# Kernel optimization log

Hardware: AMD Instinct MI355X
Metric: run time of the kernel (lower is better)

## Reference

```python
import math
import jax, jax.numpy as jnp
import numpy as np

B, S, D = 16, 2048, 256

def setup_inputs() -> dict:
    key = jax.random.key(0)
    kq, kk, kv, km = jax.random.split(key, 4)
    q = jax.random.normal(kq, (B, S, D), dtype=jnp.float32)
    k = jax.random.normal(kk, (B, S, D), dtype=jnp.float32)
    v = jax.random.normal(kv, (B, S, D), dtype=jnp.float32)
    mask = jax.random.randint(km, (B, S, S), 0, 2, dtype=jnp.int32)
    return {"q": q, "k": k, "v": v, "mask": mask}

def reference(q, k, v, mask):
    dim_input = q.shape[-1]
    # scores: [B, S, S]
    scores = jnp.einsum('bqd,bkd->bqk', q, k) / math.sqrt(dim_input)
    # non-standard masking: masked positions set to 0.0 (NOT -inf) before softmax
    scores = jnp.where(mask == 0, jnp.float32(0.0), scores)
    att = jax.nn.softmax(scores, axis=-1)
    # original: if mask.sum() == 0, attention is all zeros
    att = jnp.where(mask.sum() > 0, att, jnp.zeros_like(att))
    return jnp.einsum('bqk,bkd->bqd', att, v)
```

## Files before the change

### kernel.cpp

```cpp
#include <hip/hip_runtime.h>


#define B_  16
#define S_  2048
#define D_  256
#define KT  32
#define NT_ 64
#define TILE_BYTES 16384

typedef short bf16x8 __attribute__((ext_vector_type(8)));
typedef float f32x4  __attribute__((ext_vector_type(4)));

__device__ __forceinline__ unsigned short f2bf(float x) {
    union { float f; unsigned u; } c; c.f = x;
    unsigned u = c.u;
    u += 0x7FFFu + ((u >> 16) & 1u);
    return (unsigned short)(u >> 16);
}

#define GLDS(g, l) __builtin_amdgcn_global_load_lds( \
    (const __attribute__((address_space(1))) void*)(g), \
    (__attribute__((address_space(3))) void*)(l), 16, 0, 0)

__global__ void conv_k(const float* __restrict__ k, char* __restrict__ kbf) {
    const int gid = blockIdx.x * 256 + threadIdx.x;
    const int d8  = gid & 31;
    const int kv  = (gid >> 5) & 2047;
    const int b   = gid >> 16;
    const float* src = k + (((size_t)(b * S_ + kv)) << 8) + d8 * 8;
    const float4 f0 = *(const float4*)src;
    const float4 f1 = *(const float4*)(src + 4);
    bf16x8 h;
    h[0] = (short)f2bf(f0.x); h[1] = (short)f2bf(f0.y);
    h[2] = (short)f2bf(f0.z); h[3] = (short)f2bf(f0.w);
    h[4] = (short)f2bf(f1.x); h[5] = (short)f2bf(f1.y);
    h[6] = (short)f2bf(f1.z); h[7] = (short)f2bf(f1.w);
    const int tile = kv >> 5, kvl = kv & 31;
    char* dst = kbf + (((size_t)(b * NT_ + tile)) << 14)
                    + (kvl << 9) + ((d8 * 16) ^ ((kvl & 7) << 4));
    *(bf16x8*)dst = h;
}

__global__ void conv_vt(const float* __restrict__ v, char* __restrict__ vtbf) {
    const int gid  = blockIdx.x * 256 + threadIdx.x;
    const int d    = gid & 255;
    const int g    = (gid >> 8) & 3;
    const int tile = (gid >> 10) & 63;
    const int b    = gid >> 16;
    const int kv0  = tile * KT + g * 8;
    const float* src = v + (((size_t)(b * S_ + kv0)) << 8) + d;
    bf16x8 h;
    #pragma unroll
    for (int j = 0; j < 8; ++j) h[j] = (short)f2bf(src[(size_t)j << 8]);
    char* dst = vtbf + (((size_t)(b * NT_ + tile)) << 14)
                     + (d << 6) + ((g * 16) ^ (((d >> 1) & 3) << 4));
    *(bf16x8*)dst = h;
}

__global__ __launch_bounds__(256, 1)
void attn_main(const float* __restrict__ q, const int* __restrict__ mask,
               const char* __restrict__ kbf, const char* __restrict__ vtbf,
               float* __restrict__ out)
{
    __shared__ alignas(128) char lds[73728];

    const int tid  = threadIdx.x;
    const int wid  = tid >> 6;
    const int lane = tid & 63;
    const int ln15 = lane & 15;
    const int quad = lane >> 4;
    const int swzK = (ln15 & 7) << 4;
    const int swzA = ((ln15 >> 1) & 3) << 4;

    const int bid = blockIdx.x;
    const int bx  = (bid & 7) * 32 + (bid >> 3);
    const int b   = bx >> 4;
    const int qt  = bx & 15;
    const int qw  = qt * 128 + wid * 32;

    const float QS = 0.09016844f;
    bf16x8 aq[2][8];
    #pragma unroll
    for (int s = 0; s < 2; ++s) {
        const float* qrow = q + ((size_t)(b * S_ + qw + s * 16 + ln15)) * D_;
        #pragma unroll
        for (int ks = 0; ks < 8; ++ks) {
            const float4 f0 = *(const float4*)(qrow + ks * 32 + quad * 8);
            const float4 f1 = *(const float4*)(qrow + ks * 32 + quad * 8 + 4);
            bf16x8 a;
            a[0] = (short)f2bf(f0.x * QS); a[1] = (short)f2bf(f0.y * QS);
            a[2] = (short)f2bf(f0.z * QS); a[3] = (short)f2bf(f0.w * QS);
            a[4] = (short)f2bf(f1.x * QS); a[5] = (short)f2bf(f1.y * QS);
            a[6] = (short)f2bf(f1.z * QS); a[7] = (short)f2bf(f1.w * QS);
            aq[s][ks] = a;
        }
    }

    bf16x8 ones;
    #pragma unroll
    for (int e = 0; e < 8; ++e) ones[e] = (short)0x3F80;

    f32x4 oacc[2][16];
    #pragma unroll
    for (int s = 0; s < 2; ++s)
        #pragma unroll
        for (int i = 0; i < 16; ++i) oacc[s][i] = (f32x4){0.f, 0.f, 0.f, 0.f};
    f32x4 lacc[2];
    lacc[0] = (f32x4){0.f, 0.f, 0.f, 0.f};
    lacc[1] = (f32x4){0.f, 0.f, 0.f, 0.f};

    const char* ktile = kbf  + (((size_t)b * NT_) << 14);
    const char* vtile = vtbf + (((size_t)b * NT_) << 14);
    char* pw = lds + 65536 + wid * 2048;
    const int c0 = wid * 4;

    #pragma unroll
    for (int c = 0; c < 4; ++c) {
        GLDS(ktile + (c0 + c) * 1024 + lane * 16, lds +         (c0 + c) * 1024);
        GLDS(vtile + (c0 + c) * 1024 + lane * 16, lds + 32768 + (c0 + c) * 1024);
    }

    const int* mbase = mask + ((size_t)(b * S_ + qw + 4 * quad)) * S_;
    int mcur[16], mnext[16];
    #pragma unroll
    for (int s = 0; s < 2; ++s)
        #pragma unroll
        for (int nt = 0; nt < 2; ++nt)
            #pragma unroll
            for (int r = 0; r < 4; ++r)
                mcur[s * 8 + nt * 4 + r] =
                    mbase[(size_t)(s * 16 + r) * S_ + nt * 16 + ln15];

    for (int t = 0; t < NT_; ++t) {
        const int cur = t & 1;
        __syncthreads();

        if (t + 1 < NT_) {
            const char* kg = ktile + ((size_t)(t + 1) << 14);
            const char* vg = vtile + ((size_t)(t + 1) << 14);
            const int nb = cur ^ 1;
            #pragma unroll
            for (int c = 0; c < 4; ++c) {
                GLDS(kg + (c0 + c) * 1024 + lane * 16, lds + nb * 16384 +         (c0 + c) * 1024);
                GLDS(vg + (c0 + c) * 1024 + lane * 16, lds + 32768 + nb * 16384 + (c0 + c) * 1024);
            }
            const int kv2 = (t + 1) * KT;
            #pragma unroll
            for (int s = 0; s < 2; ++s)
                #pragma unroll
                for (int nt = 0; nt < 2; ++nt)
                    #pragma unroll
                    for (int r = 0; r < 4; ++r)
                        mnext[s * 8 + nt * 4 + r] =
                            mbase[(size_t)(s * 16 + r) * S_ + kv2 + nt * 16 + ln15];
        }

        const char* kl = lds + cur * 16384;
        f32x4 sacc[2][2];
        sacc[0][0] = (f32x4){0.f, 0.f, 0.f, 0.f};
        sacc[0][1] = (f32x4){0.f, 0.f, 0.f, 0.f};
        sacc[1][0] = (f32x4){0.f, 0.f, 0.f, 0.f};
        sacc[1][1] = (f32x4){0.f, 0.f, 0.f, 0.f};
        #pragma unroll
        for (int ks = 0; ks < 8; ++ks) {
            #pragma unroll
            for (int nt = 0; nt < 2; ++nt) {
                const int off = ((nt * 16 + ln15) << 9)
                              + (((ks << 6) + (quad << 4)) ^ swzK);
                const bf16x8 bk = *(const bf16x8*)(kl + off);
                sacc[0][nt] = __builtin_amdgcn_mfma_f32_16x16x32_bf16(aq[0][ks], bk, sacc[0][nt], 0, 0, 0);
                sacc[1][nt] = __builtin_amdgcn_mfma_f32_16x16x32_bf16(aq[1][ks], bk, sacc[1][nt], 0, 0, 0);
            }
        }

        #pragma unroll
        for (int s = 0; s < 2; ++s) {
            #pragma unroll
            for (int nt = 0; nt < 2; ++nt) {
                #pragma unroll
                for (int r = 0; r < 4; ++r) {
                    const float p = (mcur[s * 8 + nt * 4 + r] != 0)
                                  ? exp2f(sacc[s][nt][r]) : 1.0f;
                    const int row  = s * 16 + 4 * quad + r;
                    const int boff = (row << 6)
                                   + ((nt * 32 + ln15 * 2) ^ (((row >> 1) & 3) << 4));
                    *(unsigned short*)(pw + boff) = f2bf(p);
                }
            }
        }

        const bf16x8 ap0 = *(const bf16x8*)(pw + (ln15 << 6)        + ((quad << 4) ^ swzA));
        const bf16x8 ap1 = *(const bf16x8*)(pw + ((16 + ln15) << 6) + ((quad << 4) ^ swzA));
        lacc[0] = __builtin_amdgcn_mfma_f32_16x16x32_bf16(ap0, ones, lacc[0], 0, 0, 0);
        lacc[1] = __builtin_amdgcn_mfma_f32_16x16x32_bf16(ap1, ones, lacc[1], 0, 0, 0);
        const char* vl = lds + 32768 + cur * 16384;
        #pragma unroll
        for (int nt2 = 0; nt2 < 16; ++nt2) {
            const int voff = ((nt2 * 16 + ln15) << 6) + ((quad << 4) ^ swzA);
            const bf16x8 bv = *(const bf16x8*)(vl + voff);
            oacc[0][nt2] = __builtin_amdgcn_mfma_f32_16x16x32_bf16(ap0, bv, oacc[0][nt2], 0, 0, 0);
            oacc[1][nt2] = __builtin_amdgcn_mfma_f32_16x16x32_bf16(ap1, bv, oacc[1][nt2], 0, 0, 0);
        }

        if (t + 1 < NT_) {
            #pragma unroll
            for (int i = 0; i < 16; ++i) mcur[i] = mnext[i];
        }
    }

    #pragma unroll
    for (int s = 0; s < 2; ++s) {
        #pragma unroll
        for (int r = 0; r < 4; ++r) {
            const float inv = 1.0f / lacc[s][r];
            float* orow = out + ((size_t)(b * S_ + qw + s * 16 + 4 * quad + r)) * D_ + ln15;
            #pragma unroll
            for (int nt2 = 0; nt2 < 16; ++nt2)
                orow[nt2 * 16] = oacc[s][nt2][r] * inv;
        }
    }
}

#define QT 128
#define KTF 64
#define NW 8
#define KSTR 264
#define VSTR 72
#define PSTR 72

__global__ __launch_bounds__(512, 2)
void attn_fused_v1(const float* __restrict__ q, const float* __restrict__ k,
                   const float* __restrict__ v, const int* __restrict__ mask,
                   float* __restrict__ out)
{
    __shared__ unsigned short Kl[KTF * KSTR];
    __shared__ unsigned short Vt[D_ * VSTR];
    __shared__ unsigned short Pl[NW][16 * PSTR];

    const int tid  = threadIdx.x;
    const int wid  = tid >> 6;
    const int lane = tid & 63;
    const int ln15 = lane & 15;
    const int quad = lane >> 4;
    const int bid = blockIdx.x;
    const int bx  = (bid & 7) * 32 + (bid >> 3);
    const int b  = bx >> 4;
    const int qt = bx & 15;
    const int qw = qt * QT + wid * 16;

    const float* qb = q + ((size_t)b * S_ + qw) * D_;
    const float* kb = k + (size_t)b * S_ * D_;
    const float* vb = v + (size_t)b * S_ * D_;
    const int*   mb = mask + ((size_t)b * S_ + qw) * (size_t)S_;

    bf16x8 aq[8];
    {
        const float* qrow = qb + (size_t)ln15 * D_;
        #pragma unroll
        for (int ks = 0; ks < 8; ++ks) {
            const float4 f0 = *(const float4*)(qrow + ks * 32 + quad * 8);
            const float4 f1 = *(const float4*)(qrow + ks * 32 + quad * 8 + 4);
            bf16x8 a;
            a[0] = (short)f2bf(f0.x * 0.0625f); a[1] = (short)f2bf(f0.y * 0.0625f);
            a[2] = (short)f2bf(f0.z * 0.0625f); a[3] = (short)f2bf(f0.w * 0.0625f);
            a[4] = (short)f2bf(f1.x * 0.0625f); a[5] = (short)f2bf(f1.y * 0.0625f);
            a[6] = (short)f2bf(f1.z * 0.0625f); a[7] = (short)f2bf(f1.w * 0.0625f);
            aq[ks] = a;
        }
    }
    bf16x8 ones;
    #pragma unroll
    for (int e = 0; e < 8; ++e) ones[e] = (short)0x3F80;
    f32x4 oacc[16];
    #pragma unroll
    for (int i = 0; i < 16; ++i) oacc[i] = (f32x4){0.f, 0.f, 0.f, 0.f};
    f32x4 lacc = (f32x4){0.f, 0.f, 0.f, 0.f};
    const int kst_c0 = (tid & 63) * 4;

    for (int kt2 = 0; kt2 < S_ / KTF; ++kt2) {
        const int kvbase = kt2 * KTF;
        int mval[4][4];
        #pragma unroll
        for (int nt = 0; nt < 4; ++nt)
            #pragma unroll
            for (int r = 0; r < 4; ++r)
                mval[nt][r] = mb[(size_t)(4 * quad + r) * S_ + kvbase + nt * 16 + ln15];
        __syncthreads();
        {
            const float* ks_ = kb + (size_t)kvbase * D_;
            #pragma unroll
            for (int pass = 0; pass < 8; ++pass) {
                const int r = pass * 8 + wid;
                const float4 f = *(const float4*)(ks_ + (size_t)r * D_ + kst_c0);
                ushort4 h;
                h.x = f2bf(f.x); h.y = f2bf(f.y); h.z = f2bf(f.z); h.w = f2bf(f.w);
                *(ushort4*)&Kl[r * KSTR + kst_c0] = h;
            }
        }
        {
            const float* vs_ = vb + (size_t)kvbase * D_;
            #pragma unroll
            for (int pass = 0; pass < 8; ++pass) {
                const int idx = pass * 8 + wid;
                const int kv  = (idx & 3) * 16 + ln15;
                const int d0  = (idx >> 2) * 16 + 4 * quad;
                const float4 f = *(const float4*)(vs_ + (size_t)kv * D_ + d0);
                Vt[(d0 + 0) * VSTR + kv] = f2bf(f.x);
                Vt[(d0 + 1) * VSTR + kv] = f2bf(f.y);
                Vt[(d0 + 2) * VSTR + kv] = f2bf(f.z);
                Vt[(d0 + 3) * VSTR + kv] = f2bf(f.w);
            }
        }
        __syncthreads();
        f32x4 sacc[4];
        #pragma unroll
        for (int nt = 0; nt < 4; ++nt) sacc[nt] = (f32x4){0.f, 0.f, 0.f, 0.f};
        #pragma unroll
        for (int ks = 0; ks < 8; ++ks) {
            #pragma unroll
            for (int nt = 0; nt < 4; ++nt) {
                const bf16x8 bk =
                    *(const bf16x8*)&Kl[(nt * 16 + ln15) * KSTR + ks * 32 + quad * 8];
                sacc[nt] = __builtin_amdgcn_mfma_f32_16x16x32_bf16(aq[ks], bk, sacc[nt], 0, 0, 0);
            }
        }
        unsigned short* pwv = Pl[wid];
        #pragma unroll
        for (int nt = 0; nt < 4; ++nt) {
            #pragma unroll
            for (int r = 0; r < 4; ++r) {
                const float s = sacc[nt][r];
                const float p = (mval[nt][r] != 0) ? __expf(s) : 1.0f;
                pwv[(4 * quad + r) * PSTR + nt * 16 + ln15] = f2bf(p);
            }
        }
        #pragma unroll
        for (int ks2 = 0; ks2 < 2; ++ks2) {
            const bf16x8 ap = *(const bf16x8*)&pwv[ln15 * PSTR + ks2 * 32 + quad * 8];
            lacc = __builtin_amdgcn_mfma_f32_16x16x32_bf16(ap, ones, lacc, 0, 0, 0);
            #pragma unroll
            for (int nt2 = 0; nt2 < 16; ++nt2) {
                const bf16x8 bv =
                    *(const bf16x8*)&Vt[(nt2 * 16 + ln15) * VSTR + ks2 * 32 + quad * 8];
                oacc[nt2] = __builtin_amdgcn_mfma_f32_16x16x32_bf16(ap, bv, oacc[nt2], 0, 0, 0);
            }
        }
    }
    #pragma unroll
    for (int r = 0; r < 4; ++r) {
        const float inv = 1.0f / lacc[r];
        float* orow = out + ((size_t)b * S_ + qw + 4 * quad + r) * D_ + ln15;
        #pragma unroll
        for (int nt2 = 0; nt2 < 16; ++nt2)
            orow[nt2 * 16] = oacc[nt2][r] * inv;
    }
}

extern "C" void kernel_launch(void* const* d_in, const int* in_sizes, int n_in,
                              void* d_out, int out_size, void* d_ws, size_t ws_size,
                              hipStream_t stream) {
    const float* q    = (const float*)d_in[0];
    const float* k    = (const float*)d_in[1];
    const float* v    = (const float*)d_in[2];
    const int*   mask = (const int*)d_in[3];
    float*       out  = (float*)d_out;

    const size_t one = (size_t)B_ * NT_ * TILE_BYTES;
    if (ws_size >= 2 * one) {
        char* kbf  = (char*)d_ws;
        char* vtbf = kbf + one;
        conv_k <<<4096, 256, 0, stream>>>(k, kbf);
        conv_vt<<<4096, 256, 0, stream>>>(v, vtbf);
        attn_main<<<256, 256, 0, stream>>>(q, mask, kbf, vtbf, out);
    } else {
        attn_fused_v1<<<512, 512, 0, stream>>>(q, k, v, mask, out);
    }
}
```

Baseline: 182.5 us.

## Split KV tile across two wave groups with LDS reduction of partial outputs

```diff
diff --git a/kernel.cpp b/kernel.cpp
--- a/kernel.cpp
+++ b/kernel.cpp
@@ -4,9 +4,8 @@
 #define B_  16
 #define S_  2048
 #define D_  256
-#define KT  32
-#define NT_ 64
-#define TILE_BYTES 16384
+#define NPH 32
+#define TILE_BYTES 32768
 
 typedef short bf16x8 __attribute__((ext_vector_type(8)));
 typedef float f32x4  __attribute__((ext_vector_type(4)));
@@ -35,48 +34,50 @@
     h[2] = (short)f2bf(f0.z); h[3] = (short)f2bf(f0.w);
     h[4] = (short)f2bf(f1.x); h[5] = (short)f2bf(f1.y);
     h[6] = (short)f2bf(f1.z); h[7] = (short)f2bf(f1.w);
-    const int tile = kv >> 5, kvl = kv & 31;
-    char* dst = kbf + (((size_t)(b * NT_ + tile)) << 14)
+    const int tile = kv >> 6, kvl = kv & 63;
+    char* dst = kbf + (((size_t)(b * NPH + tile)) << 15)
                     + (kvl << 9) + ((d8 * 16) ^ ((kvl & 7) << 4));
     *(bf16x8*)dst = h;
 }
 
 __global__ void conv_vt(const float* __restrict__ v, char* __restrict__ vtbf) {
     const int gid  = blockIdx.x * 256 + threadIdx.x;
-    const int d    = gid & 255;
-    const int g    = (gid >> 8) & 3;
-    const int tile = (gid >> 10) & 63;
+    const int kg   = gid & 7;
+    const int d    = (gid >> 3) & 255;
+    const int tile = (gid >> 11) & 31;
     const int b    = gid >> 16;
-    const int kv0  = tile * KT + g * 8;
+    const int kv0  = tile * 64 + kg * 8;
     const float* src = v + (((size_t)(b * S_ + kv0)) << 8) + d;
     bf16x8 h;
     #pragma unroll
     for (int j = 0; j < 8; ++j) h[j] = (short)f2bf(src[(size_t)j << 8]);
-    char* dst = vtbf + (((size_t)(b * NT_ + tile)) << 14)
-                     + (d << 6) + ((g * 16) ^ (((d >> 1) & 3) << 4));
+    char* dst = vtbf + (((size_t)(b * NPH + tile)) << 15)
+                     + (d << 7) + ((kg * 16) ^ ((d & 7) << 4));
     *(bf16x8*)dst = h;
 }
 
-__global__ __launch_bounds__(256, 1)
+__global__ __launch_bounds__(512, 2)
 void attn_main(const float* __restrict__ q, const int* __restrict__ mask,
                const char* __restrict__ kbf, const char* __restrict__ vtbf,
                float* __restrict__ out)
 {
-    __shared__ alignas(128) char lds[73728];
+    __shared__ alignas(128) char lds[147456];
 
     const int tid  = threadIdx.x;
     const int wid  = tid >> 6;
     const int lane = tid & 63;
     const int ln15 = lane & 15;
     const int quad = lane >> 4;
+    const int g    = wid & 3;
+    const int h    = wid >> 2;
     const int swzK = (ln15 & 7) << 4;
-    const int swzA = ((ln15 >> 1) & 3) << 4;
+    const int swzP = ((ln15 >> 1) & 3) << 4;
 
     const int bid = blockIdx.x;
     const int bx  = (bid & 7) * 32 + (bid >> 3);
     const int b   = bx >> 4;
     const int qt  = bx & 15;
-    const int qw  = qt * 128 + wid * 32;
+    const int qw  = qt * 128 + g * 32;
 
     const float QS = 0.09016844f;
     bf16x8 aq[2][8];
@@ -109,42 +110,46 @@
     lacc[0] = (f32x4){0.f, 0.f, 0.f, 0.f};
     lacc[1] = (f32x4){0.f, 0.f, 0.f, 0.f};
 
-    const char* ktile = kbf  + (((size_t)b * NT_) << 14);
-    const char* vtile = vtbf + (((size_t)b * NT_) << 14);
-    char* pw = lds + 65536 + wid * 2048;
-    const int c0 = wid * 4;
+    const char* ktile = kbf  + (((size_t)b * NPH) << 15);
+    const char* vtile = vtbf + (((size_t)b * NPH) << 15);
+    char* pw = lds + 131072 + wid * 2048;
+    const int cK = wid * 4;
+    const int cV = wid * 4;
 
     #pragma unroll
     for (int c = 0; c < 4; ++c) {
-        GLDS(ktile + (c0 + c) * 1024 + lane * 16, lds +         (c0 + c) * 1024);
-        GLDS(vtile + (c0 + c) * 1024 + lane * 16, lds + 32768 + (c0 + c) * 1024);
+        GLDS(ktile + (cK + c) * 1024 + lane * 16, lds + (cK + c) * 1024);
+        GLDS(vtile + (cV + c) * 1024 + lane * 16, lds + 65536 + (cV + c) * 1024);
     }
 
     const int* mbase = mask + ((size_t)(b * S_ + qw + 4 * quad)) * S_;
     int mcur[16], mnext[16];
-    #pragma unroll
-    for (int s = 0; s < 2; ++s)
-        #pragma unroll
-        for (int nt = 0; nt < 2; ++nt)
-            #pragma unroll
-            for (int r = 0; r < 4; ++r)
-                mcur[s * 8 + nt * 4 + r] =
-                    mbase[(size_t)(s * 16 + r) * S_ + nt * 16 + ln15];
-
-    for (int t = 0; t < NT_; ++t) {
-        const int cur = t & 1;
+    {
+        const int kvb = h * 32;
+        #pragma unroll
+        for (int s = 0; s < 2; ++s)
+            #pragma unroll
+            for (int nt = 0; nt < 2; ++nt)
+                #pragma unroll
+                for (int r = 0; r < 4; ++r)
+                    mcur[s * 8 + nt * 4 + r] =
+                        mbase[(size_t)(s * 16 + r) * S_ + kvb + nt * 16 + ln15];
+    }
+
+    for (int ph = 0; ph < NPH; ++ph) {
+        const int cur = ph & 1;
         __syncthreads();
 
-        if (t + 1 < NT_) {
-            const char* kg = ktile + ((size_t)(t + 1) << 14);
-            const char* vg = vtile + ((size_t)(t + 1) << 14);
+        if (ph + 1 < NPH) {
+            const char* kg_ = ktile + ((size_t)(ph + 1) << 15);
+            const char* vg_ = vtile + ((size_t)(ph + 1) << 15);
             const int nb = cur ^ 1;
             #pragma unroll
             for (int c = 0; c < 4; ++c) {
-                GLDS(kg + (c0 + c) * 1024 + lane * 16, lds + nb * 16384 +         (c0 + c) * 1024);
-                GLDS(vg + (c0 + c) * 1024 + lane * 16, lds + 32768 + nb * 16384 + (c0 + c) * 1024);
-            }
-            const int kv2 = (t + 1) * KT;
+                GLDS(kg_ + (cK + c) * 1024 + lane * 16, lds + nb * 32768 + (cK + c) * 1024);
+                GLDS(vg_ + (cV + c) * 1024 + lane * 16, lds + 65536 + nb * 32768 + (cV + c) * 1024);
+            }
+            const int kv2 = (ph + 1) * 64 + h * 32;
             #pragma unroll
             for (int s = 0; s < 2; ++s)
                 #pragma unroll
@@ -155,7 +160,7 @@
                             mbase[(size_t)(s * 16 + r) * S_ + kv2 + nt * 16 + ln15];
         }
 
-        const char* kl = lds + cur * 16384;
+        const char* kl = lds + cur * 32768;
         f32x4 sacc[2][2];
         sacc[0][0] = (f32x4){0.f, 0.f, 0.f, 0.f};
         sacc[0][1] = (f32x4){0.f, 0.f, 0.f, 0.f};
@@ -165,7 +170,7 @@
         for (int ks = 0; ks < 8; ++ks) {
             #pragma unroll
             for (int nt = 0; nt < 2; ++nt) {
-                const int off = ((nt * 16 + ln15) << 9)
+                const int off = ((h * 32 + nt * 16 + ln15) << 9)
                               + (((ks << 6) + (quad << 4)) ^ swzK);
                 const bf16x8 bk = *(const bf16x8*)(kl + off);
                 sacc[0][nt] = __builtin_amdgcn_mfma_f32_16x16x32_bf16(aq[0][ks], bk, sacc[0][nt], 0, 0, 0);
@@ -189,34 +194,59 @@
             }
         }
 
-        const bf16x8 ap0 = *(const bf16x8*)(pw + (ln15 << 6)        + ((quad << 4) ^ swzA));
-        const bf16x8 ap1 = *(const bf16x8*)(pw + ((16 + ln15) << 6) + ((quad << 4) ^ swzA));
+        const bf16x8 ap0 = *(const bf16x8*)(pw + (ln15 << 6)        + ((quad << 4) ^ swzP));
+        const bf16x8 ap1 = *(const bf16x8*)(pw + ((16 + ln15) << 6) + ((quad << 4) ^ swzP));
         lacc[0] = __builtin_amdgcn_mfma_f32_16x16x32_bf16(ap0, ones, lacc[0], 0, 0, 0);
         lacc[1] = __builtin_amdgcn_mfma_f32_16x16x32_bf16(ap1, ones, lacc[1], 0, 0, 0);
-        const char* vl = lds + 32768 + cur * 16384;
+        const char* vl = lds + 65536 + cur * 32768;
         #pragma unroll
         for (int nt2 = 0; nt2 < 16; ++nt2) {
-            const int voff = ((nt2 * 16 + ln15) << 6) + ((quad << 4) ^ swzA);
+            const int voff = ((nt2 * 16 + ln15) << 7)
+                           + (((h << 6) + (quad << 4)) ^ swzK);
             const bf16x8 bv = *(const bf16x8*)(vl + voff);
             oacc[0][nt2] = __builtin_amdgcn_mfma_f32_16x16x32_bf16(ap0, bv, oacc[0][nt2], 0, 0, 0);
             oacc[1][nt2] = __builtin_amdgcn_mfma_f32_16x16x32_bf16(ap1, bv, oacc[1][nt2], 0, 0, 0);
         }
 
-        if (t + 1 < NT_) {
+        if (ph + 1 < NPH) {
             #pragma unroll
             for (int i = 0; i < 16; ++i) mcur[i] = mnext[i];
         }
     }
 
-    #pragma unroll
-    for (int s = 0; s < 2; ++s) {
-        #pragma unroll
-        for (int r = 0; r < 4; ++r) {
-            const float inv = 1.0f / lacc[s][r];
-            float* orow = out + ((size_t)(b * S_ + qw + s * 16 + 4 * quad + r)) * D_ + ln15;
-            #pragma unroll
-            for (int nt2 = 0; nt2 < 16; ++nt2)
-                orow[nt2 * 16] = oacc[s][nt2][r] * inv;
+    __syncthreads();
+    float* ob = (float*)lds;
+    float* lb = (float*)(lds + 131072);
+    if (h == 1) {
+        #pragma unroll
+        for (int s = 0; s < 2; ++s) {
+            #pragma unroll
+            for (int r = 0; r < 4; ++r)
+                lb[(g * 2 + s) * 16 + 4 * quad + r] = lacc[s][r];
+            #pragma unroll
+            for (int nt2 = 0; nt2 < 16; ++nt2) {
+                #pragma unroll
+                for (int r = 0; r < 4; ++r)
+                    ob[g * 8192 + (s * 16 + 4 * quad + r) * 256 + nt2 * 16 + ln15]
+                        = oacc[s][nt2][r];
+            }
+        }
+    }
+    __syncthreads();
+    if (h == 0) {
+        #pragma unroll
+        for (int s = 0; s < 2; ++s) {
+            #pragma unroll
+            for (int r = 0; r < 4; ++r) {
+                const float lsum = lacc[s][r] + lb[(g * 2 + s) * 16 + 4 * quad + r];
+                const float inv  = 1.0f / lsum;
+                float* orow = out + ((size_t)(b * S_ + qw + s * 16 + 4 * quad + r)) * D_ + ln15;
+                #pragma unroll
+                for (int nt2 = 0; nt2 < 16; ++nt2)
+                    orow[nt2 * 16] =
+                        (oacc[s][nt2][r]
+                         + ob[g * 8192 + (s * 16 + 4 * quad + r) * 256 + nt2 * 16 + ln15]) * inv;
+            }
         }
     }
 }
@@ -292,9 +322,9 @@
             for (int pass = 0; pass < 8; ++pass) {
                 const int r = pass * 8 + wid;
                 const float4 f = *(const float4*)(ks_ + (size_t)r * D_ + kst_c0);
-                ushort4 h;
-                h.x = f2bf(f.x); h.y = f2bf(f.y); h.z = f2bf(f.z); h.w = f2bf(f.w);
-                *(ushort4*)&Kl[r * KSTR + kst_c0] = h;
+                ushort4 hh;
+                hh.x = f2bf(f.x); hh.y = f2bf(f.y); hh.z = f2bf(f.z); hh.w = f2bf(f.w);
+                *(ushort4*)&Kl[r * KSTR + kst_c0] = hh;
             }
         }
         {
@@ -365,14 +395,14 @@
     const int*   mask = (const int*)d_in[3];
     float*       out  = (float*)d_out;
 
-    const size_t one = (size_t)B_ * NT_ * TILE_BYTES;
+    const size_t one = (size_t)B_ * NPH * TILE_BYTES;
     if (ws_size >= 2 * one) {
         char* kbf  = (char*)d_ws;
         char* vtbf = kbf + one;
         conv_k <<<4096, 256, 0, stream>>>(k, kbf);
         conv_vt<<<4096, 256, 0, stream>>>(v, vtbf);
-        attn_main<<<256, 256, 0, stream>>>(q, mask, kbf, vtbf, out);
+        attn_main<<<256, 512, 0, stream>>>(q, mask, kbf, vtbf, out);
     } else {
-        attn_fused_v1<<<512, 512, 0, stream>>>(q, k, v, mask, out);
-    }
-}
+        attn_fused_v1<<<256, 512, 0, stream>>>(q, k, v, mask, out);
+    }
+}
```

After: 225.4 us. 23.5% more time.
